# Optimization experiments

Measured on AMD Instinct MI355X. Metric: run time of the kernel, lower is better.

Reference implementation:

```python
import jax, jax.numpy as jnp
import numpy as np

M, K, O = 8192, 4096, 4096
WORDS = K // 32
INT32_MAX = 2147483647


def _unpack_ternary(nz, sgn):
    """Unpack bit-packed ternary weights.
    nz, sgn: [O, WORDS] int32 bitmasks. Bit j of word w corresponds to input
    column w*32 + j. weight = 0 if nz bit clear, else +1 (sgn bit clear) or -1.
    Returns dense float32 [O, K].
    """
    shifts = jnp.arange(32, dtype=jnp.uint32)
    nzb = (nz.astype(jnp.uint32)[:, :, None] >> shifts) & jnp.uint32(1)   # [O, WORDS, 32]
    sgb = (sgn.astype(jnp.uint32)[:, :, None] >> shifts) & jnp.uint32(1)  # [O, WORDS, 32]
    w = nzb.astype(jnp.float32) * (1.0 - 2.0 * sgb.astype(jnp.float32))
    return w.reshape(nz.shape[0], -1)  # [O, K]


def setup_inputs() -> dict:
    key = jax.random.key(0)
    k1, k2, k3, k4, k5 = jax.random.split(key, 5)
    x = jax.random.normal(k1, (M, K), dtype=jnp.float32)
    nz = jax.random.randint(k2, (O, WORDS), 0, INT32_MAX, dtype=jnp.int32)
    sgn = jax.random.randint(k3, (O, WORDS), 0, INT32_MAX, dtype=jnp.int32)
    bias = jax.random.normal(k4, (O,), dtype=jnp.float32) * 0.01
    alpha = jax.random.uniform(k5, (O,), dtype=jnp.float32, minval=0.5, maxval=1.5)
    return {"x": x, "nz": nz, "sgn": sgn, "bias": bias, "alpha": alpha}


def reference(x, nz, sgn, bias, alpha):
    # y = (x @ W^T) * alpha + bias, W dequantized from ternary bit-packs
    W = _unpack_ternary(nz, sgn)                       # [O, K]
    y = jnp.einsum('mk,ok->mo', x, W)                  # [M, O]
    y = y * alpha[None, :] + bias[None, :]
    return y
```

## Files before the change

kernel.cpp:

```cpp
#include <hip/hip_runtime.h>
#include <stdint.h>

#define M_DIM 8192
#define K_DIM 4096
#define O_DIM 4096
#define NWORDS 128

typedef __attribute__((ext_vector_type(8))) short bf16x8;
typedef __attribute__((ext_vector_type(4))) float f32x4;
typedef __attribute__((ext_vector_type(4))) float fvec4;
typedef __attribute__((ext_vector_type(4))) unsigned uvec4;
typedef __attribute__((ext_vector_type(2))) unsigned uvec2;

__device__ __forceinline__ unsigned f32_to_bf16u(float f) {
  union { float f; unsigned u; } v; v.f = f;
  return (v.u + 0x7FFFu + ((v.u >> 16) & 1u)) >> 16;
}

__device__ __forceinline__ unsigned pack_bf16x2(float lo, float hi) {
  return f32_to_bf16u(lo) | (f32_to_bf16u(hi) << 16);
}

__global__ __launch_bounds__(256) void prep_kernel(const fvec4* __restrict__ x,
                                                   uvec2* __restrict__ xb,
                                                   const unsigned* __restrict__ nz,
                                                   const unsigned* __restrict__ sgn,
                                                   unsigned short* __restrict__ wb) {
  const int b   = blockIdx.x;
  const int tid = threadIdx.x;
  if (b < 8192) {
    const long base = (long)b * 1024 + tid;
#pragma unroll
    for (int j = 0; j < 4; ++j) {
      const long g = base + j * 256;
      const fvec4 v = x[g];
      uvec2 o;
      o.x = pack_bf16x2(v.x, v.y);
      o.y = pack_bf16x2(v.z, v.w);
      xb[g] = o;
    }
  } else {
    const int i = (b - 8192) * 256 + tid;
    const int w = i >> 2;
    const int q = i & 3;
    const unsigned n = nz[w] >> (8 * q);
    const unsigned s = sgn[w] >> (8 * q);
    unsigned out[4];
#pragma unroll
    for (int p = 0; p < 4; ++p) {
      const int j0 = 2 * p, j1 = 2 * p + 1;
      unsigned lo = ((n >> j0) & 1u) ? (0x3F80u | (((s >> j0) & 1u) << 15)) : 0u;
      unsigned hi = ((n >> j1) & 1u) ? (0x3F80u | (((s >> j1) & 1u) << 15)) : 0u;
      out[p] = lo | (hi << 16);
    }
    uvec4 v = { out[0], out[1], out[2], out[3] };
    *(uvec4*)(wb + (long)w * 32 + q * 8) = v;
  }
}

__global__ __launch_bounds__(512, 2) void gemm_kernel(const unsigned short* __restrict__ A,
                                                      const unsigned short* __restrict__ B,
                                                      const float* __restrict__ bias,
                                                      const float* __restrict__ alpha,
                                                      float* __restrict__ C) {
  __shared__ unsigned short lds[65536];

  const int tid  = threadIdx.x;
  const int lane = tid & 63;
  const int wave = tid >> 6;
  const int wm   = wave >> 2;
  const int wn   = wave & 3;

  const int wg   = blockIdx.x;
  const int swz  = (wg & 7) * 64 + (wg >> 3);
  const int nBlk = (swz & 15) * 256;
  const int mBlk = (swz >> 4) * 256;

  const unsigned short* Apan = A + (long)mBlk * K_DIM;
  const unsigned short* Bpan = B + (long)nBlk * K_DIM;

  int lOff[2], gOff[2];
#pragma unroll
  for (int l = 0; l < 2; ++l) {
    const int o = (l * 512 + tid) * 16;
    const int r = o >> 7;
    const int q = ((o >> 4) & 7) ^ (r & 7);
    lOff[l] = o;
    gOff[l] = r * K_DIM + q * 8;
  }

  const int fr  = lane & 15;
  const int fq  = lane >> 4;
  const int sl0 = fq ^ (fr & 7);
  const int aFB = fr * 64;
  const int bFB = (wn & 1) * 4096 + fr * 64;
  const int A0S = wm * 8192;
  const int A1S = (2 + wm) * 8192;
  const int B0S = 32768 + (wn >> 1) * 8192;
  const int B1S = 32768 + (2 + (wn >> 1)) * 8192;

  f32x4  acc[8][4] = {};
  bf16x8 a[4][2], bv[4][2];

#define STAGE(SUBv, BUFv, TILEv) do {                                          \
    const unsigned short* s_ = (((SUBv) < 2) ? Apan : Bpan)                    \
        + (long)((SUBv) & 1) * (128 * K_DIM) + (long)(TILEv) * 64;             \
    const int dB = ((((SUBv) < 2) ? 0 : 32768)                                 \
        + (((BUFv) * 2) + ((SUBv) & 1)) * 8192) * 2;                           \
    __builtin_amdgcn_global_load_lds(                                          \
        (const __attribute__((address_space(1))) void*)(s_ + gOff[0]),         \
        (__attribute__((address_space(3))) void*)((char*)lds + dB + lOff[0]),  \
        16, 0, 0);                                                             \
    __builtin_amdgcn_global_load_lds(                                          \
        (const __attribute__((address_space(1))) void*)(s_ + gOff[1]),         \
        (__attribute__((address_space(3))) void*)((char*)lds + dB + lOff[1]),  \
        16, 0, 0);                                                             \
  } while (0)

#define LOADA(BASE, TQ)                                                        \
  _Pragma("unroll")                                                            \
  for (int i = 0; i < 4; ++i) {                                                \
    const int off_ = (BASE) + ((TQ) * 4 + i) * 1024 + aFB;                     \
    a[i][0] = *(const bf16x8*)(lds + off_ + sl0 * 8);                          \
    a[i][1] = *(const bf16x8*)(lds + off_ + (sl0 ^ 4) * 8);                    \
  }

#define LOADB(BASE)                                                            \
  _Pragma("unroll")                                                            \
  for (int j = 0; j < 4; ++j) {                                                \
    const int off_ = (BASE) + bFB + j * 1024;                                  \
    bv[j][0] = *(const bf16x8*)(lds + off_ + sl0 * 8);                         \
    bv[j][1] = *(const bf16x8*)(lds + off_ + (sl0 ^ 4) * 8);                   \
  }

#define MFMAQ(QM, QN)                                                          \
  _Pragma("unroll")                                                            \
  for (int kh = 0; kh < 2; ++kh)                                               \
    _Pragma("unroll")                                                          \
    for (int i = 0; i < 4; ++i)                                                \
      _Pragma("unroll")                                                        \
      for (int j = 0; j < 2; ++j)                                              \
        acc[(QM) * 4 + i][(QN) * 2 + j] = __builtin_amdgcn_mfma_f32_16x16x32_bf16( \
            a[i][kh], bv[(QN) * 2 + j][kh], acc[(QM) * 4 + i][(QN) * 2 + j], 0, 0, 0);

#define MID()  __builtin_amdgcn_s_barrier();                                   \
               asm volatile("s_waitcnt lgkmcnt(0)" ::: "memory");              \
               __builtin_amdgcn_s_setprio(1)
#define ENDPH()   __builtin_amdgcn_s_setprio(0); __builtin_amdgcn_s_barrier()
#define ENDVM6()  __builtin_amdgcn_s_setprio(0);                               \
                  asm volatile("s_waitcnt vmcnt(6)" ::: "memory");             \
                  __builtin_amdgcn_s_barrier()
#define ENDVM0()  __builtin_amdgcn_s_setprio(0);                               \
                  asm volatile("s_waitcnt vmcnt(0)" ::: "memory");             \
                  __builtin_amdgcn_s_barrier()

  STAGE(2, 0, 0); STAGE(3, 0, 0); STAGE(0, 0, 0); STAGE(1, 0, 0);
  STAGE(2, 1, 1); STAGE(3, 1, 1); STAGE(0, 1, 1);
  asm volatile("s_waitcnt vmcnt(6)" ::: "memory");
  __builtin_amdgcn_s_barrier();

  for (int it = 0; it < (K_DIM / 64) / 2 - 1; ++it) {
    const int t1 = 2 * it + 1, t2 = 2 * it + 2, t3 = 2 * it + 3;
    LOADA(A0S, 0); LOADB(B0S); STAGE(1, 1, t1); MID(); MFMAQ(0, 0); ENDPH();
                               STAGE(2, 0, t2); MID(); MFMAQ(0, 1); ENDPH();
    LOADA(A0S, 1);             STAGE(3, 0, t2); MID(); MFMAQ(1, 0); ENDPH();
                               STAGE(0, 0, t2); MID(); MFMAQ(1, 1); ENDVM6();
    LOADA(A1S, 0); LOADB(B1S); STAGE(1, 0, t2); MID(); MFMAQ(0, 0); ENDPH();
                               STAGE(2, 1, t3); MID(); MFMAQ(0, 1); ENDPH();
    LOADA(A1S, 1);             STAGE(3, 1, t3); MID(); MFMAQ(1, 0); ENDPH();
                               STAGE(0, 1, t3); MID(); MFMAQ(1, 1); ENDVM6();
  }

  LOADA(A0S, 0); LOADB(B0S); STAGE(1, 1, 63); MID(); MFMAQ(0, 0); ENDPH();
                                              MID(); MFMAQ(0, 1); ENDPH();
  LOADA(A0S, 1);                              MID(); MFMAQ(1, 0); ENDPH();
                                              MID(); MFMAQ(1, 1); ENDVM0();
  LOADA(A1S, 0); LOADB(B1S);                  MID(); MFMAQ(0, 0); ENDPH();
                                              MID(); MFMAQ(0, 1); ENDPH();
  LOADA(A1S, 1);                              MID(); MFMAQ(1, 0); ENDPH();
                                              MID(); MFMAQ(1, 1);
  __builtin_amdgcn_s_setprio(0);

#pragma unroll
  for (int tn = 0; tn < 4; ++tn) {
    const int n = nBlk + wn * 64 + tn * 16 + fr;
    const float al = alpha[n];
    const float bi = bias[n];
#pragma unroll
    for (int tm = 0; tm < 8; ++tm) {
      const int mBase = mBlk + wm * 128 + tm * 16 + fq * 4;
#pragma unroll
      for (int r = 0; r < 4; ++r)
        __builtin_nontemporal_store(acc[tm][tn][r] * al + bi,
                                    C + (long)(mBase + r) * O_DIM + n);
    }
  }

#undef STAGE
#undef LOADA
#undef LOADB
#undef MFMAQ
#undef MID
#undef ENDPH
#undef ENDVM6
#undef ENDVM0
}

__global__ __launch_bounds__(256) void fallback_kernel(const float* __restrict__ x,
                                                       const unsigned* __restrict__ nz,
                                                       const unsigned* __restrict__ sgn,
                                                       const float* __restrict__ bias,
                                                       const float* __restrict__ alpha,
                                                       float* __restrict__ y) {
  long gid = (long)blockIdx.x * 256 + threadIdx.x;
  int o = (int)(gid % O_DIM);
  long m = gid / O_DIM;
  const float* xr = x + m * K_DIM;
  float s = 0.f;
  for (int w = 0; w < NWORDS; ++w) {
    unsigned n = nz[o * NWORDS + w];
    unsigned g = sgn[o * NWORDS + w];
    for (int j = 0; j < 32; ++j) {
      if ((n >> j) & 1u) {
        float v = xr[w * 32 + j];
        s += ((g >> j) & 1u) ? -v : v;
      }
    }
  }
  y[gid] = s * alpha[o] + bias[o];
}

extern "C" void kernel_launch(void* const* d_in, const int* in_sizes, int n_in,
                              void* d_out, int out_size, void* d_ws, size_t ws_size,
                              hipStream_t stream) {
  const float*    x     = (const float*)d_in[0];
  const unsigned* nz    = (const unsigned*)d_in[1];
  const unsigned* sgn   = (const unsigned*)d_in[2];
  const float*    bias  = (const float*)d_in[3];
  const float*    alpha = (const float*)d_in[4];
  float*          y     = (float*)d_out;

  const size_t xb_bytes = (size_t)M_DIM * K_DIM * 2;
  const size_t wb_bytes = (size_t)O_DIM * K_DIM * 2;

  if (ws_size >= xb_bytes + wb_bytes) {
    unsigned short* xb = (unsigned short*)d_ws;
    unsigned short* wb = (unsigned short*)((char*)d_ws + xb_bytes);

    prep_kernel<<<16384, 256, 0, stream>>>((const fvec4*)x, (uvec2*)xb, nz, sgn, wb);
    gemm_kernel<<<512, 512, 0, stream>>>(xb, wb, bias, alpha, y);
  } else {
    fallback_kernel<<<(long)M_DIM * O_DIM / 256, 256, 0, stream>>>(x, nz, sgn, bias, alpha, y);
  }
}
```

Before: 436.9 us.

## Rework GEMM phase schedule into four A-row passes and grid-stride prep kernel

```diff
diff --git a/kernel.cpp b/kernel.cpp
--- a/kernel.cpp
+++ b/kernel.cpp
@@ -10,7 +10,6 @@
 typedef __attribute__((ext_vector_type(4))) float f32x4;
 typedef __attribute__((ext_vector_type(4))) float fvec4;
 typedef __attribute__((ext_vector_type(4))) unsigned uvec4;
-typedef __attribute__((ext_vector_type(2))) unsigned uvec2;
 
 __device__ __forceinline__ unsigned f32_to_bf16u(float f) {
   union { float f; unsigned u; } v; v.f = f;
@@ -22,39 +21,40 @@
 }
 
 __global__ __launch_bounds__(256) void prep_kernel(const fvec4* __restrict__ x,
-                                                   uvec2* __restrict__ xb,
+                                                   uvec4* __restrict__ xb4,
                                                    const unsigned* __restrict__ nz,
                                                    const unsigned* __restrict__ sgn,
                                                    unsigned short* __restrict__ wb) {
   const int b   = blockIdx.x;
   const int tid = threadIdx.x;
-  if (b < 8192) {
-    const long base = (long)b * 1024 + tid;
-#pragma unroll
-    for (int j = 0; j < 4; ++j) {
-      const long g = base + j * 256;
-      const fvec4 v = x[g];
-      uvec2 o;
-      o.x = pack_bf16x2(v.x, v.y);
-      o.y = pack_bf16x2(v.z, v.w);
-      xb[g] = o;
+  if (b < 2048) {
+    for (long p = (long)b * 256 + tid; p < 4194304; p += 524288) {
+      const fvec4 v0 = x[2 * p];
+      const fvec4 v1 = x[2 * p + 1];
+      uvec4 o;
+      o.x = pack_bf16x2(v0.x, v0.y);
+      o.y = pack_bf16x2(v0.z, v0.w);
+      o.z = pack_bf16x2(v1.x, v1.y);
+      o.w = pack_bf16x2(v1.z, v1.w);
+      xb4[p] = o;
     }
   } else {
-    const int i = (b - 8192) * 256 + tid;
-    const int w = i >> 2;
-    const int q = i & 3;
-    const unsigned n = nz[w] >> (8 * q);
-    const unsigned s = sgn[w] >> (8 * q);
-    unsigned out[4];
-#pragma unroll
-    for (int p = 0; p < 4; ++p) {
-      const int j0 = 2 * p, j1 = 2 * p + 1;
-      unsigned lo = ((n >> j0) & 1u) ? (0x3F80u | (((s >> j0) & 1u) << 15)) : 0u;
-      unsigned hi = ((n >> j1) & 1u) ? (0x3F80u | (((s >> j1) & 1u) << 15)) : 0u;
-      out[p] = lo | (hi << 16);
-    }
-    uvec4 v = { out[0], out[1], out[2], out[3] };
-    *(uvec4*)(wb + (long)w * 32 + q * 8) = v;
+    for (long i = (long)(b - 2048) * 256 + tid; i < 2097152; i += 131072) {
+      const int w = (int)(i >> 2);
+      const int q = (int)(i & 3);
+      const unsigned n = nz[w] >> (8 * q);
+      const unsigned s = sgn[w] >> (8 * q);
+      unsigned out[4];
+#pragma unroll
+      for (int pq = 0; pq < 4; ++pq) {
+        const int j0 = 2 * pq, j1 = 2 * pq + 1;
+        unsigned lo = ((n >> j0) & 1u) ? (0x3F80u | (((s >> j0) & 1u) << 15)) : 0u;
+        unsigned hi = ((n >> j1) & 1u) ? (0x3F80u | (((s >> j1) & 1u) << 15)) : 0u;
+        out[pq] = lo | (hi << 16);
+      }
+      uvec4 v = { out[0], out[1], out[2], out[3] };
+      *(uvec4*)(wb + (long)w * 32 + q * 8) = v;
+    }
   }
 }
 
@@ -100,7 +100,7 @@
   const int B1S = 32768 + (2 + (wn >> 1)) * 8192;
 
   f32x4  acc[8][4] = {};
-  bf16x8 a[4][2], bv[4][2];
+  bf16x8 a[2][2], bv[4][2];
 
 #define STAGE(SUBv, BUFv, TILEv) do {                                          \
     const unsigned short* s_ = (((SUBv) < 2) ? Apan : Bpan)                    \
@@ -117,10 +117,10 @@
         16, 0, 0);                                                             \
   } while (0)
 
-#define LOADA(BASE, TQ)                                                        \
+#define LOADA2(BASE, P)                                                        \
   _Pragma("unroll")                                                            \
-  for (int i = 0; i < 4; ++i) {                                                \
-    const int off_ = (BASE) + ((TQ) * 4 + i) * 1024 + aFB;                     \
+  for (int i = 0; i < 2; ++i) {                                                \
+    const int off_ = (BASE) + ((P) * 2 + i) * 1024 + aFB;                      \
     a[i][0] = *(const bf16x8*)(lds + off_ + sl0 * 8);                          \
     a[i][1] = *(const bf16x8*)(lds + off_ + (sl0 ^ 4) * 8);                    \
   }
@@ -133,52 +133,56 @@
     bv[j][1] = *(const bf16x8*)(lds + off_ + (sl0 ^ 4) * 8);                   \
   }
 
-#define MFMAQ(QM, QN)                                                          \
+#define MFMA2(P)                                                               \
   _Pragma("unroll")                                                            \
   for (int kh = 0; kh < 2; ++kh)                                               \
     _Pragma("unroll")                                                          \
-    for (int i = 0; i < 4; ++i)                                                \
+    for (int i = 0; i < 2; ++i)                                                \
       _Pragma("unroll")                                                        \
-      for (int j = 0; j < 2; ++j)                                              \
-        acc[(QM) * 4 + i][(QN) * 2 + j] = __builtin_amdgcn_mfma_f32_16x16x32_bf16( \
-            a[i][kh], bv[(QN) * 2 + j][kh], acc[(QM) * 4 + i][(QN) * 2 + j], 0, 0, 0);
-
+      for (int tn = 0; tn < 4; ++tn)                                           \
+        acc[(P) * 2 + i][tn] = __builtin_amdgcn_mfma_f32_16x16x32_bf16(        \
+            a[i][kh], bv[tn][kh], acc[(P) * 2 + i][tn], 0, 0, 0);
+
+#define PRE12()   asm volatile("s_waitcnt lgkmcnt(8)" ::: "memory")
 #define MID()  __builtin_amdgcn_s_barrier();                                   \
                asm volatile("s_waitcnt lgkmcnt(0)" ::: "memory");              \
                __builtin_amdgcn_s_setprio(1)
 #define ENDPH()   __builtin_amdgcn_s_setprio(0); __builtin_amdgcn_s_barrier()
-#define ENDVM6()  __builtin_amdgcn_s_setprio(0);                               \
-                  asm volatile("s_waitcnt vmcnt(6)" ::: "memory");             \
+#define ENDVM4()  __builtin_amdgcn_s_setprio(0);                               \
+                  asm volatile("s_waitcnt vmcnt(4)" ::: "memory");             \
                   __builtin_amdgcn_s_barrier()
 #define ENDVM0()  __builtin_amdgcn_s_setprio(0);                               \
                   asm volatile("s_waitcnt vmcnt(0)" ::: "memory");             \
                   __builtin_amdgcn_s_barrier()
 
   STAGE(2, 0, 0); STAGE(3, 0, 0); STAGE(0, 0, 0); STAGE(1, 0, 0);
-  STAGE(2, 1, 1); STAGE(3, 1, 1); STAGE(0, 1, 1);
-  asm volatile("s_waitcnt vmcnt(6)" ::: "memory");
+  STAGE(2, 1, 1); STAGE(3, 1, 1);
+  asm volatile("s_waitcnt vmcnt(4)" ::: "memory");
   __builtin_amdgcn_s_barrier();
 
   for (int it = 0; it < (K_DIM / 64) / 2 - 1; ++it) {
     const int t1 = 2 * it + 1, t2 = 2 * it + 2, t3 = 2 * it + 3;
-    LOADA(A0S, 0); LOADB(B0S); STAGE(1, 1, t1); MID(); MFMAQ(0, 0); ENDPH();
-                               STAGE(2, 0, t2); MID(); MFMAQ(0, 1); ENDPH();
-    LOADA(A0S, 1);             STAGE(3, 0, t2); MID(); MFMAQ(1, 0); ENDPH();
-                               STAGE(0, 0, t2); MID(); MFMAQ(1, 1); ENDVM6();
-    LOADA(A1S, 0); LOADB(B1S); STAGE(1, 0, t2); MID(); MFMAQ(0, 0); ENDPH();
-                               STAGE(2, 1, t3); MID(); MFMAQ(0, 1); ENDPH();
-    LOADA(A1S, 1);             STAGE(3, 1, t3); MID(); MFMAQ(1, 0); ENDPH();
-                               STAGE(0, 1, t3); MID(); MFMAQ(1, 1); ENDVM6();
-  }
-
-  LOADA(A0S, 0); LOADB(B0S); STAGE(1, 1, 63); MID(); MFMAQ(0, 0); ENDPH();
-                                              MID(); MFMAQ(0, 1); ENDPH();
-  LOADA(A0S, 1);                              MID(); MFMAQ(1, 0); ENDPH();
-                                              MID(); MFMAQ(1, 1); ENDVM0();
-  LOADA(A1S, 0); LOADB(B1S);                  MID(); MFMAQ(0, 0); ENDPH();
-                                              MID(); MFMAQ(0, 1); ENDPH();
-  LOADA(A1S, 1);                              MID(); MFMAQ(1, 0); ENDPH();
-                                              MID(); MFMAQ(1, 1);
+    LOADA2(A0S, 0); LOADB(B0S); STAGE(1, 1, t1); PRE12();
+                                                 MID(); MFMA2(0); ENDPH();
+    LOADA2(A0S, 1);             STAGE(0, 1, t1); MID(); MFMA2(1); ENDPH();
+    LOADA2(A0S, 2);             STAGE(2, 0, t2); MID(); MFMA2(2); ENDPH();
+    LOADA2(A0S, 3);             STAGE(3, 0, t2); MID(); MFMA2(3); ENDVM4();
+    LOADA2(A1S, 0); LOADB(B1S); STAGE(0, 0, t2); PRE12();
+                                                 MID(); MFMA2(0); ENDPH();
+    LOADA2(A1S, 1);             STAGE(1, 0, t2); MID(); MFMA2(1); ENDPH();
+    LOADA2(A1S, 2);             STAGE(2, 1, t3); MID(); MFMA2(2); ENDPH();
+    LOADA2(A1S, 3);             STAGE(3, 1, t3); MID(); MFMA2(3); ENDVM4();
+  }
+
+  LOADA2(A0S, 0); LOADB(B0S); STAGE(1, 1, 63); PRE12();
+                                               MID(); MFMA2(0); ENDPH();
+  LOADA2(A0S, 1);             STAGE(0, 1, 63); MID(); MFMA2(1); ENDPH();
+  LOADA2(A0S, 2);                              MID(); MFMA2(2); ENDPH();
+  LOADA2(A0S, 3);                              MID(); MFMA2(3); ENDVM0();
+  LOADA2(A1S, 0); LOADB(B1S);                  MID(); MFMA2(0); ENDPH();
+  LOADA2(A1S, 1);                              MID(); MFMA2(1); ENDPH();
+  LOADA2(A1S, 2);                              MID(); MFMA2(2); ENDPH();
+  LOADA2(A1S, 3);                              MID(); MFMA2(3);
   __builtin_amdgcn_s_setprio(0);
 
 #pragma unroll
@@ -197,12 +201,13 @@
   }
 
 #undef STAGE
-#undef LOADA
+#undef LOADA2
 #undef LOADB
-#undef MFMAQ
+#undef MFMA2
+#undef PRE12
 #undef MID
 #undef ENDPH
-#undef ENDVM6
+#undef ENDVM4
 #undef ENDVM0
 }
 
@@ -247,7 +252,7 @@
     unsigned short* xb = (unsigned short*)d_ws;
     unsigned short* wb = (unsigned short*)((char*)d_ws + xb_bytes);
 
-    prep_kernel<<<16384, 256, 0, stream>>>((const fvec4*)x, (uvec2*)xb, nz, sgn, wb);
+    prep_kernel<<<2560, 256, 0, stream>>>((const fvec4*)x, (uvec4*)xb, nz, sgn, wb);
     gemm_kernel<<<512, 512, 0, stream>>>(xb, wb, bias, alpha, y);
   } else {
     fallback_kernel<<<(long)M_DIM * O_DIM / 256, 256, 0, stream>>>(x, nz, sgn, bias, alpha, y);
```

Result: no change. 435.3 us (-0.4%).
